# Optimization experiments

Measured on AMD Instinct MI355X. Metric: run time of the kernel, lower is better.

The kernel has to match this reference:

```python
import jax, jax.numpy as jnp
import numpy as np

TEMPERATURE = 0.04
EPS = 1e-6

def _conv_valid(x, k, groups=1):
    # x: [N,C,H,W], k: [O,I,kh,kw]
    return jax.lax.conv_general_dilated(
        x, k, window_strides=(1, 1), padding='VALID',
        dimension_numbers=('NCHW', 'OIHW', 'NCHW'),
        feature_group_count=groups)

def setup_inputs() -> dict:
    key = jax.random.key(0)
    k1, k2 = jax.random.split(key)
    roi_piece = jax.random.normal(k1, (256, 1, 17, 17), dtype=jnp.float32)
    roi_background = jax.random.normal(k2, (256, 1, 384, 384), dtype=jnp.float32)
    return {"roi_piece": roi_piece, "roi_background": roi_background}

def reference(roi_piece, roi_background):
    B, _, Ht, Wt = roi_piece.shape
    Hi, Wi = roi_background.shape[-2:]
    Lh, Lw = Hi - Ht + 1, Wi - Wt + 1
    n = Ht * Wt

    # --- template normalization (torch .std is unbiased, ddof=1) ---
    t = roi_piece - jnp.mean(roi_piece, axis=(2, 3), keepdims=True)
    t_std = jnp.maximum(jnp.sqrt(jnp.var(t, axis=(2, 3), keepdims=True, ddof=1)), EPS)
    t_norm = t / t_std  # [B,1,Ht,Wt], zero-mean per batch

    # --- fast ZNCC: since sum(t_norm)==0, corr = corr(image, t_norm) / window_std ---
    # per-batch cross-correlation via grouped conv: batch -> channels/groups
    num = _conv_valid(roi_background.reshape(1, B, Hi, Wi), t_norm, groups=B)[0]  # [B,Lh,Lw]

    # sliding-window mean/var via box filters (var unbiased=False, clamped then sqrt)
    ones_k = jnp.ones((1, 1, Ht, Wt), dtype=roi_background.dtype)
    s1 = _conv_valid(roi_background, ones_k)        # [B,1,Lh,Lw]
    s2 = _conv_valid(roi_background * roi_background, ones_k)
    mu = s1 / n
    var = jnp.maximum(s2 / n - mu * mu, EPS)
    std = jnp.sqrt(var)[:, 0]                        # [B,Lh,Lw]

    corr = num / std  # [B,Lh,Lw]

    # --- soft-argmax over the correlation map ---
    probs = jax.nn.softmax(corr.reshape(B, -1) / TEMPERATURE, axis=-1).reshape(B, Lh, Lw)
    y_coords = jnp.arange(Lh, dtype=corr.dtype)
    x_coords = jnp.arange(Lw, dtype=corr.dtype)
    expected_y = jnp.einsum('bhw,h->b', probs, y_coords)
    expected_x = jnp.einsum('bhw,w->b', probs, x_coords)
    offset_y = expected_y - (Lh - 1) / 2.0
    offset_x = expected_x - (Lw - 1) / 2.0
    offset = jnp.stack([offset_x, offset_y], axis=1)  # [B,2]

    max_corr = jnp.max(corr, axis=(1, 2))             # [B]
    return offset, max_corr
```

## Files before the change

kernel.cpp:

```cpp
#include <hip/hip_runtime.h>
#include <math.h>

#define NB 256
#define HT 17
#define WT 17
#define HI 384
#define WI 384
#define LH 368
#define LW 368
#define NTEMPL 289
#define TPAD 20
#define TY 32
#define TX 64
#define NTXT 6
#define NTYT 12
#define NTILES 72
#define BR 48
#define BP 84
#define TEMP_INV 25.0f
#define EPSV 1e-6f

__global__ __launch_bounds__(256) void tmpl_norm_kernel(
    const float* __restrict__ piece, float* __restrict__ tn) {
    int b = blockIdx.x;
    const float* x = piece + b * NTEMPL;
    int tid = threadIdx.x;
    int wid = tid >> 6, lane = tid & 63;

    float v0 = (tid < NTEMPL) ? x[tid] : 0.f;
    float v1 = (tid + 256 < NTEMPL) ? x[tid + 256] : 0.f;

    __shared__ float sred[4];
    float s = v0 + v1;
    #pragma unroll
    for (int o = 32; o > 0; o >>= 1) s += __shfl_down(s, o, 64);
    if (lane == 0) sred[wid] = s;
    __syncthreads();
    float mean = (sred[0] + sred[1] + sred[2] + sred[3]) * (1.0f / NTEMPL);

    float d0 = (tid < NTEMPL) ? (v0 - mean) : 0.f;
    float d1 = (tid + 256 < NTEMPL) ? (v1 - mean) : 0.f;
    float q = d0 * d0 + d1 * d1;
    __syncthreads();
    #pragma unroll
    for (int o = 32; o > 0; o >>= 1) q += __shfl_down(q, o, 64);
    if (lane == 0) sred[wid] = q;
    __syncthreads();
    float var = (sred[0] + sred[1] + sred[2] + sred[3]) * (1.0f / (NTEMPL - 1));
    float stdv = sqrtf(var);
    if (stdv < EPSV) stdv = EPSV;
    float inv = 1.0f / stdv;

    float* o = tn + b * (HT * TPAD);
    for (int sIdx = tid; sIdx < HT * TPAD; sIdx += 256) {
        int i = sIdx / TPAD, j = sIdx % TPAD;
        o[sIdx] = (j < WT) ? (x[i * WT + j] - mean) * inv : 0.f;
    }
}

template<int P, bool LAST>
__device__ __forceinline__ void corr_step(
    int i, int tr2, int xb,
    const float* __restrict__ tp,
    const float (*__restrict__ bg)[BP],
    float (&bbf)[2][TPAD], float (&ttf)[2][TPAD], float (&acc)[2][4])
{
    if (!LAST) {
        const float4* tq = (const float4*)(tp + (i + 1) * TPAD);
        #pragma unroll
        for (int q = 0; q < 5; ++q) ((float4*)ttf[P ^ 1])[q] = tq[q];
    }
    const float* tc = ttf[P];
    #pragma unroll
    for (int j = 0; j < 17; ++j) {
        float tv = tc[j];
        #pragma unroll
        for (int k = 0; k < 4; ++k) acc[0][k] = fmaf(tv, bbf[P][j + k], acc[0][k]);
    }
    if (!LAST) {
        const float4* br = (const float4*)&bg[tr2 + i + 2][xb];
        #pragma unroll
        for (int q = 0; q < 5; ++q) ((float4*)bbf[P])[q] = br[q];
    }
    #pragma unroll
    for (int j = 0; j < 17; ++j) {
        float tv = tc[j];
        #pragma unroll
        for (int k = 0; k < 4; ++k) acc[1][k] = fmaf(tv, bbf[P ^ 1][j + k], acc[1][k]);
    }
}

__global__ __launch_bounds__(256, 4) void corr_kernel(
    const float* __restrict__ bgg, const float* __restrict__ tn,
    float* __restrict__ partials) {
    int blk = blockIdx.x;
    int b = blk / NTILES;
    int t = blk % NTILES;
    int ty0 = (t / NTXT) * TY;
    int tx0 = (t % NTXT) * TX;
    const float* img = bgg + (size_t)b * HI * WI;
    const float* tp  = tn + b * (HT * TPAD);

    __shared__ float bg[BR][BP];
    __shared__ float c1[TY][BP];
    __shared__ float c2[TY][BP];
    __shared__ float redm[4], redl[4], redy[4], redx[4];

    int tid = threadIdx.x;
    int wid = tid >> 6, lane = tid & 63;

    for (int l = tid; l < BR * (BP / 4); l += 256) {
        int r = l / (BP / 4), c = (l % (BP / 4)) * 4;
        int iy = ty0 + r, ix = tx0 + c;
        float4 v = make_float4(0.f, 0.f, 0.f, 0.f);
        if (iy < HI && ix < WI) v = *(const float4*)(img + iy * WI + ix);
        *(float4*)&bg[r][c] = v;
    }
    __syncthreads();

    if (tid < 160) {
        int cc = tid % 80, r0 = (tid / 80) * 16;
        float s = 0.f, s2 = 0.f;
        #pragma unroll
        for (int i2 = 0; i2 < HT; ++i2) { float v = bg[r0 + i2][cc]; s += v; s2 = fmaf(v, v, s2); }
        c1[r0][cc] = s; c2[r0][cc] = s2;
        for (int r = r0 + 1; r < r0 + 16; ++r) {
            float vn = bg[r + 16][cc], vo = bg[r - 1][cc];
            s += vn - vo; s2 += vn * vn - vo * vo;
            c1[r][cc] = s; c2[r][cc] = s2;
        }
    }
    __syncthreads();

    int tr2 = (tid >> 4) * 2;
    int xb  = (tid & 15) * 4;
    float bbf[2][TPAD];
    float ttf[2][TPAD];
    float acc[2][4] = {};

    #pragma unroll
    for (int m = 0; m < 2; ++m) {
        const float4* br = (const float4*)&bg[tr2 + m][xb];
        #pragma unroll
        for (int q = 0; q < 5; ++q) ((float4*)bbf[m])[q] = br[q];
    }
    {
        const float4* t0 = (const float4*)tp;
        #pragma unroll
        for (int q = 0; q < 5; ++q) ((float4*)ttf[0])[q] = t0[q];
    }

    for (int i = 0; i < 16; i += 2) {
        corr_step<0, false>(i,     tr2, xb, tp, bg, bbf, ttf, acc);
        corr_step<1, false>(i + 1, tr2, xb, tp, bg, bbf, ttf, acc);
    }
    corr_step<0, true>(16, tr2, xb, tp, bg, bbf, ttf, acc);

    const float invn = 1.0f / NTEMPL;
    float corr[2][4];
    float m = -INFINITY;
    #pragma unroll
    for (int e = 0; e < 2; ++e) {
        float cc1f[TPAD], cc2f[TPAD];
        const float4* a1 = (const float4*)&c1[tr2 + e][xb];
        const float4* a2 = (const float4*)&c2[tr2 + e][xb];
        #pragma unroll
        for (int q = 0; q < 5; ++q) { ((float4*)cc1f)[q] = a1[q]; ((float4*)cc2f)[q] = a2[q]; }
        float s1 = 0.f, s2 = 0.f;
        #pragma unroll
        for (int j = 0; j < HT; ++j) { s1 += cc1f[j]; s2 += cc2f[j]; }
        int oy = ty0 + tr2 + e;
        #pragma unroll
        for (int k = 0; k < 4; ++k) {
            float mu = s1 * invn;
            float var = s2 * invn - mu * mu;
            if (var < EPSV) var = EPSV;
            float cv = acc[e][k] / sqrtf(var);
            int ox = tx0 + xb + k;
            if (oy < LH && ox < LW) m = fmaxf(m, cv);
            else cv = -INFINITY;
            corr[e][k] = cv;
            if (k < 3) {
                s1 += cc1f[k + HT] - cc1f[k];
                s2 += cc2f[k + HT] - cc2f[k];
            }
        }
    }

    float mm = m;
    #pragma unroll
    for (int o = 32; o > 0; o >>= 1) mm = fmaxf(mm, __shfl_down(mm, o, 64));
    if (lane == 0) redm[wid] = mm;
    __syncthreads();
    float M = fmaxf(fmaxf(redm[0], redm[1]), fmaxf(redm[2], redm[3]));

    float l = 0.f, sy = 0.f, sx = 0.f;
    #pragma unroll
    for (int e = 0; e < 2; ++e) {
        int oy = ty0 + tr2 + e;
        #pragma unroll
        for (int k = 0; k < 4; ++k) {
            float cv = corr[e][k];
            float ev = (cv == -INFINITY) ? 0.f : __expf((cv - M) * TEMP_INV);
            l += ev;
            sy = fmaf(ev, (float)oy, sy);
            sx = fmaf(ev, (float)(tx0 + xb + k), sx);
        }
    }
    #pragma unroll
    for (int o = 32; o > 0; o >>= 1) {
        l  += __shfl_down(l, o, 64);
        sy += __shfl_down(sy, o, 64);
        sx += __shfl_down(sx, o, 64);
    }
    if (lane == 0) { redl[wid] = l; redy[wid] = sy; redx[wid] = sx; }
    __syncthreads();
    if (tid == 0) {
        float* p = partials + (size_t)blk * 4;
        p[0] = M;
        p[1] = redl[0] + redl[1] + redl[2] + redl[3];
        p[2] = redy[0] + redy[1] + redy[2] + redy[3];
        p[3] = redx[0] + redx[1] + redx[2] + redx[3];
    }
}

__global__ __launch_bounds__(256) void reduce_kernel(
    const float* __restrict__ partials, float* __restrict__ out) {
    int b = blockIdx.x;
    int tid = threadIdx.x;
    int wid = tid >> 6, lane = tid & 63;

    float m = -INFINITY, l = 0.f, sy = 0.f, sx = 0.f;
    if (tid < NTILES) {
        const float* p = partials + (size_t)(b * NTILES + tid) * 4;
        m = p[0]; l = p[1]; sy = p[2]; sx = p[3];
    }
    __shared__ float rm[4], rl[4], ry[4], rx[4];
    float mm = m;
    #pragma unroll
    for (int o = 32; o > 0; o >>= 1) mm = fmaxf(mm, __shfl_down(mm, o, 64));
    if (lane == 0) rm[wid] = mm;
    __syncthreads();
    float M = fmaxf(fmaxf(rm[0], rm[1]), fmaxf(rm[2], rm[3]));

    float sc = (m == -INFINITY) ? 0.f : __expf((m - M) * TEMP_INV);
    l *= sc; sy *= sc; sx *= sc;
    #pragma unroll
    for (int o = 32; o > 0; o >>= 1) {
        l  += __shfl_down(l, o, 64);
        sy += __shfl_down(sy, o, 64);
        sx += __shfl_down(sx, o, 64);
    }
    if (lane == 0) { rl[wid] = l; ry[wid] = sy; rx[wid] = sx; }
    __syncthreads();
    if (tid == 0) {
        float L  = rl[0] + rl[1] + rl[2] + rl[3];
        float SY = ry[0] + ry[1] + ry[2] + ry[3];
        float SX = rx[0] + rx[1] + rx[2] + rx[3];
        out[b * 2 + 0] = SX / L - 183.5f;
        out[b * 2 + 1] = SY / L - 183.5f;
        out[2 * NB + b] = M;
    }
}

extern "C" void kernel_launch(void* const* d_in, const int* in_sizes, int n_in,
                              void* d_out, int out_size, void* d_ws, size_t ws_size,
                              hipStream_t stream) {
    const float* piece = (const float*)d_in[0];
    const float* bgg   = (const float*)d_in[1];
    float* out = (float*)d_out;

    float* tn = (float*)d_ws;
    float* partials = tn + NB * HT * TPAD;

    tmpl_norm_kernel<<<NB, 256, 0, stream>>>(piece, tn);
    corr_kernel<<<NB * NTILES, 256, 0, stream>>>(bgg, tn, partials);
    reduce_kernel<<<NB, 256, 0, stream>>>(partials, out);
}
```

Measured before the change: 533.7 us.

## Enlarge correlation tile to 32x128 and compute 4x4 outputs per thread

The correlation tile widens from 64 to 128 columns, which halves the block count. Each thread now computes 4 output rows by 4 columns, with a 4-deep rotating register window of background rows, so every template row loaded from memory is reused across 4 output rows. This is meant to cut per-output LDS and global template loads and the halo overhead. In exchange the kernel needs more registers and a larger LDS footprint (launch_bounds drops to 2 blocks per SM), and a single wave of fewer, bigger blocks may lower occupancy and load balance.

```diff
diff --git a/kernel.cpp b/kernel.cpp
--- a/kernel.cpp
+++ b/kernel.cpp
@@ -11,12 +11,12 @@
 #define NTEMPL 289
 #define TPAD 20
 #define TY 32
-#define TX 64
-#define NTXT 6
+#define TX 128
+#define NTXT 3
 #define NTYT 12
-#define NTILES 72
+#define NTILES 36
 #define BR 48
-#define BP 84
+#define BP 144
 #define TEMP_INV 25.0f
 #define EPSV 1e-6f
 
@@ -60,37 +60,41 @@
 
 template<int P, bool LAST>
 __device__ __forceinline__ void corr_step(
-    int i, int tr2, int xb,
+    int i, int tr, int xb,
     const float* __restrict__ tp,
     const float (*__restrict__ bg)[BP],
-    float (&bbf)[2][TPAD], float (&ttf)[2][TPAD], float (&acc)[2][4])
+    float (&w)[4][TPAD], float (&ttf)[2][TPAD], float (&acc)[4][4])
 {
     if (!LAST) {
         const float4* tq = (const float4*)(tp + (i + 1) * TPAD);
         #pragma unroll
-        for (int q = 0; q < 5; ++q) ((float4*)ttf[P ^ 1])[q] = tq[q];
-    }
-    const float* tc = ttf[P];
+        for (int q = 0; q < 5; ++q) ((float4*)ttf[(P & 1) ^ 1])[q] = tq[q];
+    }
+    const float* tc = ttf[P & 1];
     #pragma unroll
     for (int j = 0; j < 17; ++j) {
         float tv = tc[j];
         #pragma unroll
-        for (int k = 0; k < 4; ++k) acc[0][k] = fmaf(tv, bbf[P][j + k], acc[0][k]);
+        for (int k = 0; k < 4; ++k) acc[0][k] = fmaf(tv, w[P][j + k], acc[0][k]);
     }
     if (!LAST) {
-        const float4* br = (const float4*)&bg[tr2 + i + 2][xb];
-        #pragma unroll
-        for (int q = 0; q < 5; ++q) ((float4*)bbf[P])[q] = br[q];
-    }
-    #pragma unroll
-    for (int j = 0; j < 17; ++j) {
-        float tv = tc[j];
-        #pragma unroll
-        for (int k = 0; k < 4; ++k) acc[1][k] = fmaf(tv, bbf[P ^ 1][j + k], acc[1][k]);
-    }
-}
-
-__global__ __launch_bounds__(256, 4) void corr_kernel(
+        const float4* br = (const float4*)&bg[tr + i + 4][xb];
+        #pragma unroll
+        for (int q = 0; q < 5; ++q) ((float4*)w[P])[q] = br[q];
+    }
+    #pragma unroll
+    for (int e = 1; e < 4; ++e) {
+        #pragma unroll
+        for (int j = 0; j < 17; ++j) {
+            float tv = tc[j];
+            #pragma unroll
+            for (int k = 0; k < 4; ++k)
+                acc[e][k] = fmaf(tv, w[(P + e) & 3][j + k], acc[e][k]);
+        }
+    }
+}
+
+__global__ __launch_bounds__(256, 2) void corr_kernel(
     const float* __restrict__ bgg, const float* __restrict__ tn,
     float* __restrict__ partials) {
     int blk = blockIdx.x;
@@ -118,8 +122,10 @@
     }
     __syncthreads();
 
-    if (tid < 160) {
-        int cc = tid % 80, r0 = (tid / 80) * 16;
+    for (int task = tid; task < 2 * BP; task += 256) {
+        int half = (task >= BP) ? 1 : 0;
+        int cc = task - half * BP;
+        int r0 = half * 16;
         float s = 0.f, s2 = 0.f;
         #pragma unroll
         for (int i2 = 0; i2 < HT; ++i2) { float v = bg[r0 + i2][cc]; s += v; s2 = fmaf(v, v, s2); }
@@ -132,17 +138,17 @@
     }
     __syncthreads();
 
-    int tr2 = (tid >> 4) * 2;
-    int xb  = (tid & 15) * 4;
-    float bbf[2][TPAD];
+    int tr = (tid >> 5) * 4;
+    int xb = (tid & 31) * 4;
+    float w[4][TPAD];
     float ttf[2][TPAD];
-    float acc[2][4] = {};
-
-    #pragma unroll
-    for (int m = 0; m < 2; ++m) {
-        const float4* br = (const float4*)&bg[tr2 + m][xb];
-        #pragma unroll
-        for (int q = 0; q < 5; ++q) ((float4*)bbf[m])[q] = br[q];
+    float acc[4][4] = {};
+
+    #pragma unroll
+    for (int m = 0; m < 4; ++m) {
+        const float4* br = (const float4*)&bg[tr + m][xb];
+        #pragma unroll
+        for (int q = 0; q < 5; ++q) ((float4*)w[m])[q] = br[q];
     }
     {
         const float4* t0 = (const float4*)tp;
@@ -150,26 +156,28 @@
         for (int q = 0; q < 5; ++q) ((float4*)ttf[0])[q] = t0[q];
     }
 
-    for (int i = 0; i < 16; i += 2) {
-        corr_step<0, false>(i,     tr2, xb, tp, bg, bbf, ttf, acc);
-        corr_step<1, false>(i + 1, tr2, xb, tp, bg, bbf, ttf, acc);
-    }
-    corr_step<0, true>(16, tr2, xb, tp, bg, bbf, ttf, acc);
+    for (int i = 0; i < 16; i += 4) {
+        corr_step<0, false>(i,     tr, xb, tp, bg, w, ttf, acc);
+        corr_step<1, false>(i + 1, tr, xb, tp, bg, w, ttf, acc);
+        corr_step<2, false>(i + 2, tr, xb, tp, bg, w, ttf, acc);
+        corr_step<3, false>(i + 3, tr, xb, tp, bg, w, ttf, acc);
+    }
+    corr_step<0, true>(16, tr, xb, tp, bg, w, ttf, acc);
 
     const float invn = 1.0f / NTEMPL;
-    float corr[2][4];
+    float corr[4][4];
     float m = -INFINITY;
     #pragma unroll
-    for (int e = 0; e < 2; ++e) {
+    for (int e = 0; e < 4; ++e) {
         float cc1f[TPAD], cc2f[TPAD];
-        const float4* a1 = (const float4*)&c1[tr2 + e][xb];
-        const float4* a2 = (const float4*)&c2[tr2 + e][xb];
+        const float4* a1 = (const float4*)&c1[tr + e][xb];
+        const float4* a2 = (const float4*)&c2[tr + e][xb];
         #pragma unroll
         for (int q = 0; q < 5; ++q) { ((float4*)cc1f)[q] = a1[q]; ((float4*)cc2f)[q] = a2[q]; }
         float s1 = 0.f, s2 = 0.f;
         #pragma unroll
         for (int j = 0; j < HT; ++j) { s1 += cc1f[j]; s2 += cc2f[j]; }
-        int oy = ty0 + tr2 + e;
+        int oy = ty0 + tr + e;
         #pragma unroll
         for (int k = 0; k < 4; ++k) {
             float mu = s1 * invn;
@@ -196,8 +204,8 @@
 
     float l = 0.f, sy = 0.f, sx = 0.f;
     #pragma unroll
-    for (int e = 0; e < 2; ++e) {
-        int oy = ty0 + tr2 + e;
+    for (int e = 0; e < 4; ++e) {
+        int oy = ty0 + tr + e;
         #pragma unroll
         for (int k = 0; k < 4; ++k) {
             float cv = corr[e][k];
```

Measured after the change: 519.7 us. 1.03x faster.
